# Optimization experiments

Hardware: AMD Instinct MI355X
Metric: run time of the kernel (lower is better)

Reference implementation:

```python
import jax, jax.numpy as jnp
import numpy as np

N = 62          # EEG channels (nodes per graph)
B = 512         # graphs in batch
K = 2           # SGConv propagation steps
F_IN = 128
H = 64
C = 3


def _complete_graph_edge_index():
    # edge e = g*N*N + i*N + j connects node g*N+i -> g*N+j,
    # matching edge_weight = Wsym.reshape(-1).repeat(B) ordering.
    base = np.arange(N)
    ii = np.tile(np.repeat(base, N), B)
    jj = np.tile(np.tile(base, N), B)
    off = np.repeat(np.arange(B) * N, N * N)
    return jnp.asarray(np.stack([off + ii, off + jj]).astype(np.int32))


def setup_inputs() -> dict:
    key = jax.random.key(0)
    ks = jax.random.split(key, 6)
    n_total = B * N
    x = jax.random.normal(ks[0], (n_total, F_IN), dtype=jnp.float32)
    edge_weight_tril = jax.random.normal(ks[1], (N * (N + 1) // 2,), dtype=jnp.float32)
    W1 = jax.random.normal(ks[2], (H, F_IN), dtype=jnp.float32) * (1.0 / np.sqrt(F_IN))
    b1 = jax.random.normal(ks[3], (H,), dtype=jnp.float32) * 0.01
    W2 = jax.random.normal(ks[4], (C, H), dtype=jnp.float32) * (1.0 / np.sqrt(H))
    b2 = jax.random.normal(ks[5], (C,), dtype=jnp.float32) * 0.01
    edge_index = _complete_graph_edge_index()
    batch = jnp.asarray(np.repeat(np.arange(B), N).astype(np.int32))
    return {"x": x, "edge_weight_tril": edge_weight_tril, "W1": W1, "b1": b1,
            "W2": W2, "b2": b2, "edge_index": edge_index, "batch": batch,
            "batch_size": B}


def reference(x, edge_weight_tril, W1, b1, W2, b2, edge_index, batch, batch_size):
    n_total = x.shape[0]
    # rebuild symmetric dense adjacency from lower-tri params
    xs, ys = np.tril_indices(N)
    Wm = jnp.zeros((N, N), dtype=x.dtype).at[xs, ys].set(edge_weight_tril)
    Wsym = Wm + Wm.T - jnp.diag(jnp.diag(Wm))
    ew = jnp.tile(Wsym.reshape(-1), batch_size)            # [B*N*N]

    row, col = edge_index[0], edge_index[1]
    # symmetric normalization (graph already contains self loops)
    deg = jax.ops.segment_sum(jnp.abs(ew), row, num_segments=n_total)
    dinv = jnp.where(deg > 0, deg ** -0.5, 0.0)
    norm = dinv[row] * ew * dinv[col]                      # [E]

    # K-step SGConv propagation: gather, scale, scatter-add
    h = x
    for _ in range(K):
        h = jax.ops.segment_sum(norm[:, None] * h[row], col, num_segments=n_total)

    h = jax.nn.relu(h @ W1.T + b1)                         # [n_total, H]
    pooled = jax.ops.segment_sum(h, batch, num_segments=batch_size)  # global_add_pool
    latent_v = pooled                                      # dropout in eval mode = identity
    logits = latent_v @ W2.T + b2
    logp = jax.nn.log_softmax(logits, axis=-1)
    return latent_v, logp
```

## Files before the change

### kernel.cpp

```cpp
#include <hip/hip_runtime.h>
#include <math.h>

#define NN  62
#define BGR 512
#define FIN 128
#define HD  64
#define NC  3

#define FMA4(dd, ss, vv) { (dd).x += (ss)*(vv).x; (dd).y += (ss)*(vv).y; (dd).z += (ss)*(vv).z; (dd).w += (ss)*(vv).w; }
#define RELUACC(pp, qq) { (pp).x += fmaxf((qq).x,0.f); (pp).y += fmaxf((qq).y,0.f); (pp).z += fmaxf((qq).z,0.f); (pp).w += fmaxf((qq).w,0.f); }


__global__ __launch_bounds__(256) void prep_kernel(const float* __restrict__ tril,
                                                   const float* __restrict__ W1,
                                                   float* __restrict__ A2g,
                                                   float* __restrict__ W1T) {
    __shared__ float LDSU[128 * 129];
    const int t = threadIdx.x;
    const int b = blockIdx.x;

    if (b == 4) {
        for (int e = t; e < HD * FIN; e += 256) {
            int h = e >> 7, f = e & 127;
            LDSU[h * 129 + f] = W1[e];
        }
        __syncthreads();
        for (int e = t; e < FIN * HD; e += 256) {
            int f = e >> 6, h = e & 63;
            W1T[e] = LDSU[h * 129 + f];
        }
        return;
    }

    float* trilS = LDSU;
    float* dinv  = LDSU + 1984;
    float* Ac    = LDSU + 2048;

    for (int e = t; e < NN * (NN + 1) / 2; e += 256) trilS[e] = tril[e];
    __syncthreads();
    if (t < NN) {
        float s = 0.f;
        for (int j = 0; j < NN; ++j) {
            int hi = max(t, j), lo = min(t, j);
            s += fabsf(trilS[hi * (hi + 1) / 2 + lo]);
        }
        dinv[t] = (s > 0.f) ? (1.0f / sqrtf(s)) : 0.f;
    }
    __syncthreads();
    for (int e = t; e < 64 * 64; e += 256) {
        int i = e >> 6, j = e & 63;
        float v = 0.f;
        if (i < NN && j < NN) {
            int hi = max(i, j), lo = min(i, j);
            v = dinv[i] * trilS[hi * (hi + 1) / 2 + lo] * dinv[j];
        }
        Ac[e] = v;
    }
    __syncthreads();
    {
        const int il = t >> 4, j4 = t & 15;
        const int i = 16 * b + il;
        const float4* Ac4 = (const float4*)Ac;
        float4 s4 = {0.f, 0.f, 0.f, 0.f};
        for (int k = 0; k < NN; ++k) {
            float a = Ac[i * 64 + k];
            float4 av = Ac4[k * 16 + j4];
            FMA4(s4, a, av);
        }
        ((float4*)A2g)[i * 16 + j4] = s4;
    }
}

__global__ __launch_bounds__(256) void gcn_fused(
    const float* __restrict__ x, const float* __restrict__ A2g,
    const float* __restrict__ W1T, const float* __restrict__ b1,
    const float* __restrict__ W2, const float* __restrict__ b2,
    float* __restrict__ out) {
    __shared__ float Xs[64 * 132];
    __shared__ float WU[128 * 64];

    const int t = threadIdx.x;
    const int g = blockIdx.x;
    const int iq = t >> 4;
    const int hq = t & 15;

    float4* Xs4 = (float4*)Xs;
    float4* WU4 = (float4*)WU;
    const float4* xg4  = (const float4*)(x + (size_t)g * NN * FIN);
    const float4* w1t4 = (const float4*)W1T;

    for (int e = t; e < 2048; e += 256) {
        int row = e >> 5, f4 = e & 31;
        float4 v = {0.f, 0.f, 0.f, 0.f};
        if (e < NN * 32) v = xg4[e];
        Xs4[row * 33 + f4] = v;
    }
    for (int e = t; e < 2048; e += 256) WU4[e] = w1t4[e];
    __syncthreads();

    float4 acc0 = {0,0,0,0}, acc1 = {0,0,0,0}, acc2 = {0,0,0,0}, acc3 = {0,0,0,0};
    for (int f4 = 0; f4 < 32; ++f4) {
        float4 xv0 = Xs4[(iq     ) * 33 + f4];
        float4 xv1 = Xs4[(iq + 16) * 33 + f4];
        float4 xv2 = Xs4[(iq + 32) * 33 + f4];
        float4 xv3 = Xs4[(iq + 48) * 33 + f4];
        float4 wv0 = WU4[(4 * f4 + 0) * 16 + hq];
        float4 wv1 = WU4[(4 * f4 + 1) * 16 + hq];
        float4 wv2 = WU4[(4 * f4 + 2) * 16 + hq];
        float4 wv3 = WU4[(4 * f4 + 3) * 16 + hq];
        FMA4(acc0, xv0.x, wv0); FMA4(acc0, xv0.y, wv1); FMA4(acc0, xv0.z, wv2); FMA4(acc0, xv0.w, wv3);
        FMA4(acc1, xv1.x, wv0); FMA4(acc1, xv1.y, wv1); FMA4(acc1, xv1.z, wv2); FMA4(acc1, xv1.w, wv3);
        FMA4(acc2, xv2.x, wv0); FMA4(acc2, xv2.y, wv1); FMA4(acc2, xv2.z, wv2); FMA4(acc2, xv2.w, wv3);
        FMA4(acc3, xv3.x, wv0); FMA4(acc3, xv3.y, wv1); FMA4(acc3, xv3.z, wv2); FMA4(acc3, xv3.w, wv3);
    }
    __syncthreads();

    float4* Yt4 = Xs4;
    Yt4[hq * 65 + iq     ] = acc0;
    Yt4[hq * 65 + iq + 16] = acc1;
    Yt4[hq * 65 + iq + 32] = acc2;
    Yt4[hq * 65 + iq + 48] = acc3;
    const float4* a2g4 = (const float4*)A2g;
    for (int e = t; e < 1024; e += 256) {
        int row = e >> 4, k4 = e & 15;
        WU4[row * 17 + k4] = a2g4[e];
    }
    __syncthreads();

    float4 b1v = ((const float4*)b1)[hq];
    float4 z0 = b1v, z1 = b1v, z2 = b1v, z3 = b1v;
    for (int j4 = 0; j4 < 16; ++j4) {
        float4 a0 = WU4[(iq     ) * 17 + j4];
        float4 a1 = WU4[(iq + 16) * 17 + j4];
        float4 a2 = WU4[(iq + 32) * 17 + j4];
        float4 a3 = WU4[(iq + 48) * 17 + j4];
        float4 y0 = Yt4[hq * 65 + 4 * j4 + 0];
        float4 y1 = Yt4[hq * 65 + 4 * j4 + 1];
        float4 y2 = Yt4[hq * 65 + 4 * j4 + 2];
        float4 y3 = Yt4[hq * 65 + 4 * j4 + 3];
        FMA4(z0, a0.x, y0); FMA4(z0, a0.y, y1); FMA4(z0, a0.z, y2); FMA4(z0, a0.w, y3);
        FMA4(z1, a1.x, y0); FMA4(z1, a1.y, y1); FMA4(z1, a1.z, y2); FMA4(z1, a1.w, y3);
        FMA4(z2, a2.x, y0); FMA4(z2, a2.y, y1); FMA4(z2, a2.z, y2); FMA4(z2, a2.w, y3);
        FMA4(z3, a3.x, y0); FMA4(z3, a3.y, y1); FMA4(z3, a3.z, y2); FMA4(z3, a3.w, y3);
    }

    float4 p = {0.f, 0.f, 0.f, 0.f};
    RELUACC(p, z0);
    RELUACC(p, z1);
    RELUACC(p, z2);
    if (iq < 14) RELUACC(p, z3);
    float* Pr = WU + 4352;
    Pr[(4 * hq + 0) * 17 + iq] = p.x;
    Pr[(4 * hq + 1) * 17 + iq] = p.y;
    Pr[(4 * hq + 2) * 17 + iq] = p.z;
    Pr[(4 * hq + 3) * 17 + iq] = p.w;
    __syncthreads();

    float* pooledS = WU + 5504;
    if (t < HD) {
        float s = 0.f;
        for (int q = 0; q < 16; ++q) s += Pr[t * 17 + q];
        out[(size_t)g * HD + t] = s;
        pooledS[t] = s;
    }
    __syncthreads();

    if (t < NC) {
        float lg[NC];
#pragma unroll
        for (int c = 0; c < NC; ++c) {
            float zz = b2[c];
            for (int h = 0; h < HD; ++h) zz += pooledS[h] * W2[c * HD + h];
            lg[c] = zz;
        }
        float m = fmaxf(lg[0], fmaxf(lg[1], lg[2]));
        float lse = m + logf(expf(lg[0] - m) + expf(lg[1] - m) + expf(lg[2] - m));
        out[(size_t)BGR * HD + (size_t)g * NC + t] = lg[t] - lse;
    }
}

extern "C" void kernel_launch(void* const* d_in, const int* in_sizes, int n_in,
                              void* d_out, int out_size, void* d_ws, size_t ws_size,
                              hipStream_t stream) {
    const float* x    = (const float*)d_in[0];
    const float* tril = (const float*)d_in[1];
    const float* W1   = (const float*)d_in[2];
    const float* b1   = (const float*)d_in[3];
    const float* W2   = (const float*)d_in[4];
    const float* b2   = (const float*)d_in[5];
    float* out  = (float*)d_out;
    float* A2g  = (float*)d_ws;
    float* W1T  = (float*)d_ws + 4096;

    prep_kernel<<<5, 256, 0, stream>>>(tril, W1, A2g, W1T);
    gcn_fused<<<BGR, 256, 0, stream>>>(x, A2g, W1T, b1, W2, b2, out);
}
```

Baseline: 106.2 us.

## Use bf16 split-precision MFMA for both per-graph matmuls

```diff
diff --git a/kernel.cpp b/kernel.cpp
--- a/kernel.cpp
+++ b/kernel.cpp
@@ -7,34 +7,43 @@
 #define HD  64
 #define NC  3
 
-#define FMA4(dd, ss, vv) { (dd).x += (ss)*(vv).x; (dd).y += (ss)*(vv).y; (dd).z += (ss)*(vv).z; (dd).w += (ss)*(vv).w; }
-#define RELUACC(pp, qq) { (pp).x += fmaxf((qq).x,0.f); (pp).y += fmaxf((qq).y,0.f); (pp).z += fmaxf((qq).z,0.f); (pp).w += fmaxf((qq).w,0.f); }
+typedef __attribute__((ext_vector_type(8))) short          bf16x8;
+typedef __attribute__((ext_vector_type(4))) float          f32x4;
+typedef __attribute__((ext_vector_type(4))) unsigned short us4;
+
+static __device__ __forceinline__ unsigned short f2bf(float f) {
+    union { float f; unsigned u; } v; v.f = f;
+    unsigned u = v.u;
+    return (unsigned short)((u + 0x7fffu + ((u >> 16) & 1u)) >> 16);
+}
+static __device__ __forceinline__ float bf2f(unsigned short h) {
+    union { unsigned u; float f; } v; v.u = ((unsigned)h) << 16;
+    return v.f;
+}
 
 
 __global__ __launch_bounds__(256) void prep_kernel(const float* __restrict__ tril,
                                                    const float* __restrict__ W1,
-                                                   float* __restrict__ A2g,
-                                                   float* __restrict__ W1T) {
-    __shared__ float LDSU[128 * 129];
+                                                   unsigned short* __restrict__ wsu) {
+    __shared__ float LDSF[1984 + 64 + 4096];
     const int t = threadIdx.x;
     const int b = blockIdx.x;
 
     if (b == 4) {
         for (int e = t; e < HD * FIN; e += 256) {
             int h = e >> 7, f = e & 127;
-            LDSU[h * 129 + f] = W1[e];
-        }
-        __syncthreads();
-        for (int e = t; e < FIN * HD; e += 256) {
-            int f = e >> 6, h = e & 63;
-            W1T[e] = LDSU[h * 129 + f];
+            float w = W1[e];
+            unsigned short hi = f2bf(w);
+            unsigned short lo = f2bf(w - bf2f(hi));
+            wsu[9216  + h * 136 + f] = hi;
+            wsu[17920 + h * 136 + f] = lo;
         }
         return;
     }
 
-    float* trilS = LDSU;
-    float* dinv  = LDSU + 1984;
-    float* Ac    = LDSU + 2048;
+    float* trilS = LDSF;
+    float* dinv  = LDSF + 1984;
+    float* Ac    = LDSF + 2048;
 
     for (int e = t; e < NN * (NN + 1) / 2; e += 256) trilS[e] = tril[e];
     __syncthreads();
@@ -65,101 +74,134 @@
         for (int k = 0; k < NN; ++k) {
             float a = Ac[i * 64 + k];
             float4 av = Ac4[k * 16 + j4];
-            FMA4(s4, a, av);
-        }
-        ((float4*)A2g)[i * 16 + j4] = s4;
+            s4.x += a * av.x; s4.y += a * av.y; s4.z += a * av.z; s4.w += a * av.w;
+        }
+        us4 hh, ll;
+        hh[0] = f2bf(s4.x); ll[0] = f2bf(s4.x - bf2f(hh[0]));
+        hh[1] = f2bf(s4.y); ll[1] = f2bf(s4.y - bf2f(hh[1]));
+        hh[2] = f2bf(s4.z); ll[2] = f2bf(s4.z - bf2f(hh[2]));
+        hh[3] = f2bf(s4.w); ll[3] = f2bf(s4.w - bf2f(hh[3]));
+        *(us4*)&wsu[       i * 72 + 4 * j4] = hh;
+        *(us4*)&wsu[4608 + i * 72 + 4 * j4] = ll;
     }
 }
 
 __global__ __launch_bounds__(256) void gcn_fused(
-    const float* __restrict__ x, const float* __restrict__ A2g,
-    const float* __restrict__ W1T, const float* __restrict__ b1,
-    const float* __restrict__ W2, const float* __restrict__ b2,
-    float* __restrict__ out) {
-    __shared__ float Xs[64 * 132];
-    __shared__ float WU[128 * 64];
+    const float* __restrict__ x, const unsigned short* __restrict__ wsu,
+    const float* __restrict__ b1, const float* __restrict__ W2,
+    const float* __restrict__ b2, float* __restrict__ out) {
+    __shared__ unsigned short SH[34816];
+    __shared__ float TAIL[64 * 17 + 64 + 64];
+    float* partial = TAIL;
+    float* pooledS = TAIL + 1088;
+    float* b1S     = TAIL + 1152;
 
     const int t = threadIdx.x;
     const int g = blockIdx.x;
-    const int iq = t >> 4;
-    const int hq = t & 15;
-
-    float4* Xs4 = (float4*)Xs;
-    float4* WU4 = (float4*)WU;
-    const float4* xg4  = (const float4*)(x + (size_t)g * NN * FIN);
-    const float4* w1t4 = (const float4*)W1T;
-
+    const int lane = t & 63, wv = t >> 6, quad = lane >> 4, l15 = lane & 15;
+
+    if (t < 16) *(float4*)&b1S[4 * t] = ((const float4*)b1)[t];
+
+    const float4* xg4 = (const float4*)(x + (size_t)g * NN * FIN);
     for (int e = t; e < 2048; e += 256) {
-        int row = e >> 5, f4 = e & 31;
+        int row = e >> 5, k4 = e & 31;
         float4 v = {0.f, 0.f, 0.f, 0.f};
-        if (e < NN * 32) v = xg4[e];
-        Xs4[row * 33 + f4] = v;
-    }
-    for (int e = t; e < 2048; e += 256) WU4[e] = w1t4[e];
-    __syncthreads();
-
-    float4 acc0 = {0,0,0,0}, acc1 = {0,0,0,0}, acc2 = {0,0,0,0}, acc3 = {0,0,0,0};
-    for (int f4 = 0; f4 < 32; ++f4) {
-        float4 xv0 = Xs4[(iq     ) * 33 + f4];
-        float4 xv1 = Xs4[(iq + 16) * 33 + f4];
-        float4 xv2 = Xs4[(iq + 32) * 33 + f4];
-        float4 xv3 = Xs4[(iq + 48) * 33 + f4];
-        float4 wv0 = WU4[(4 * f4 + 0) * 16 + hq];
-        float4 wv1 = WU4[(4 * f4 + 1) * 16 + hq];
-        float4 wv2 = WU4[(4 * f4 + 2) * 16 + hq];
-        float4 wv3 = WU4[(4 * f4 + 3) * 16 + hq];
-        FMA4(acc0, xv0.x, wv0); FMA4(acc0, xv0.y, wv1); FMA4(acc0, xv0.z, wv2); FMA4(acc0, xv0.w, wv3);
-        FMA4(acc1, xv1.x, wv0); FMA4(acc1, xv1.y, wv1); FMA4(acc1, xv1.z, wv2); FMA4(acc1, xv1.w, wv3);
-        FMA4(acc2, xv2.x, wv0); FMA4(acc2, xv2.y, wv1); FMA4(acc2, xv2.z, wv2); FMA4(acc2, xv2.w, wv3);
-        FMA4(acc3, xv3.x, wv0); FMA4(acc3, xv3.y, wv1); FMA4(acc3, xv3.z, wv2); FMA4(acc3, xv3.w, wv3);
-    }
-    __syncthreads();
-
-    float4* Yt4 = Xs4;
-    Yt4[hq * 65 + iq     ] = acc0;
-    Yt4[hq * 65 + iq + 16] = acc1;
-    Yt4[hq * 65 + iq + 32] = acc2;
-    Yt4[hq * 65 + iq + 48] = acc3;
-    const float4* a2g4 = (const float4*)A2g;
-    for (int e = t; e < 1024; e += 256) {
-        int row = e >> 4, k4 = e & 15;
-        WU4[row * 17 + k4] = a2g4[e];
-    }
-    __syncthreads();
-
-    float4 b1v = ((const float4*)b1)[hq];
-    float4 z0 = b1v, z1 = b1v, z2 = b1v, z3 = b1v;
-    for (int j4 = 0; j4 < 16; ++j4) {
-        float4 a0 = WU4[(iq     ) * 17 + j4];
-        float4 a1 = WU4[(iq + 16) * 17 + j4];
-        float4 a2 = WU4[(iq + 32) * 17 + j4];
-        float4 a3 = WU4[(iq + 48) * 17 + j4];
-        float4 y0 = Yt4[hq * 65 + 4 * j4 + 0];
-        float4 y1 = Yt4[hq * 65 + 4 * j4 + 1];
-        float4 y2 = Yt4[hq * 65 + 4 * j4 + 2];
-        float4 y3 = Yt4[hq * 65 + 4 * j4 + 3];
-        FMA4(z0, a0.x, y0); FMA4(z0, a0.y, y1); FMA4(z0, a0.z, y2); FMA4(z0, a0.w, y3);
-        FMA4(z1, a1.x, y0); FMA4(z1, a1.y, y1); FMA4(z1, a1.z, y2); FMA4(z1, a1.w, y3);
-        FMA4(z2, a2.x, y0); FMA4(z2, a2.y, y1); FMA4(z2, a2.z, y2); FMA4(z2, a2.w, y3);
-        FMA4(z3, a3.x, y0); FMA4(z3, a3.y, y1); FMA4(z3, a3.z, y2); FMA4(z3, a3.w, y3);
-    }
-
-    float4 p = {0.f, 0.f, 0.f, 0.f};
-    RELUACC(p, z0);
-    RELUACC(p, z1);
-    RELUACC(p, z2);
-    if (iq < 14) RELUACC(p, z3);
-    float* Pr = WU + 4352;
-    Pr[(4 * hq + 0) * 17 + iq] = p.x;
-    Pr[(4 * hq + 1) * 17 + iq] = p.y;
-    Pr[(4 * hq + 2) * 17 + iq] = p.z;
-    Pr[(4 * hq + 3) * 17 + iq] = p.w;
-    __syncthreads();
-
-    float* pooledS = WU + 5504;
+        if (e < 1984) v = xg4[e];
+        us4 hh, ll;
+        hh[0] = f2bf(v.x); ll[0] = f2bf(v.x - bf2f(hh[0]));
+        hh[1] = f2bf(v.y); ll[1] = f2bf(v.y - bf2f(hh[1]));
+        hh[2] = f2bf(v.z); ll[2] = f2bf(v.z - bf2f(hh[2]));
+        hh[3] = f2bf(v.w); ll[3] = f2bf(v.w - bf2f(hh[3]));
+        *(us4*)&SH[       row * 136 + k4 * 4] = hh;
+        *(us4*)&SH[8704 + row * 136 + k4 * 4] = ll;
+    }
+    {
+        const float4* wsrc = (const float4*)(wsu + 9216);
+        for (int e = t; e < 2176; e += 256) *(float4*)&SH[17408 + e * 8] = wsrc[e];
+    }
+    __syncthreads();
+
+    f32x4 y0 = {0,0,0,0}, y1 = {0,0,0,0}, y2 = {0,0,0,0}, y3 = {0,0,0,0};
+    {
+        const int arow = (16 * wv + l15) * 136 + quad * 8;
+#pragma unroll
+        for (int c = 0; c < 4; ++c) {
+            bf16x8 ahi = *(bf16x8*)&SH[arow + c * 32];
+            bf16x8 alo = *(bf16x8*)&SH[8704 + arow + c * 32];
+#define P1TILE(ACC, NT) { \
+            int bo = (16 * NT + l15) * 136 + quad * 8 + c * 32; \
+            bf16x8 bhi = *(bf16x8*)&SH[17408 + bo]; \
+            bf16x8 blo = *(bf16x8*)&SH[26112 + bo]; \
+            ACC = __builtin_amdgcn_mfma_f32_16x16x32_bf16(ahi, bhi, ACC, 0, 0, 0); \
+            ACC = __builtin_amdgcn_mfma_f32_16x16x32_bf16(ahi, blo, ACC, 0, 0, 0); \
+            ACC = __builtin_amdgcn_mfma_f32_16x16x32_bf16(alo, bhi, ACC, 0, 0, 0); \
+            ACC = __builtin_amdgcn_mfma_f32_16x16x32_bf16(alo, blo, ACC, 0, 0, 0); }
+            P1TILE(y0, 0) P1TILE(y1, 1) P1TILE(y2, 2) P1TILE(y3, 3)
+#undef P1TILE
+        }
+    }
+    __syncthreads();
+
+    {
+        const int mbase = 16 * wv + quad * 4;
+#define YTW(ACC, NT) { \
+        int n = 16 * NT + l15; \
+        us4 hh, ll; \
+        hh[0] = f2bf(ACC[0]); ll[0] = f2bf(ACC[0] - bf2f(hh[0])); \
+        hh[1] = f2bf(ACC[1]); ll[1] = f2bf(ACC[1] - bf2f(hh[1])); \
+        hh[2] = f2bf(ACC[2]); ll[2] = f2bf(ACC[2] - bf2f(hh[2])); \
+        hh[3] = f2bf(ACC[3]); ll[3] = f2bf(ACC[3] - bf2f(hh[3])); \
+        *(us4*)&SH[       n * 72 + mbase] = hh; \
+        *(us4*)&SH[4608 + n * 72 + mbase] = ll; }
+        YTW(y0, 0) YTW(y1, 1) YTW(y2, 2) YTW(y3, 3)
+#undef YTW
+    }
+    {
+        const float4* a2src = (const float4*)wsu;
+        for (int e = t; e < 1152; e += 256) *(float4*)&SH[9216 + e * 8] = a2src[e];
+    }
+    __syncthreads();
+
+    f32x4 z0 = {0,0,0,0}, z1 = {0,0,0,0}, z2 = {0,0,0,0}, z3 = {0,0,0,0};
+    {
+        const int arow = 9216 + (16 * wv + l15) * 72 + quad * 8;
+#pragma unroll
+        for (int c = 0; c < 2; ++c) {
+            bf16x8 ahi = *(bf16x8*)&SH[arow + c * 32];
+            bf16x8 alo = *(bf16x8*)&SH[4608 + arow + c * 32];
+#define P2TILE(ACC, NT) { \
+            int bo = (16 * NT + l15) * 72 + quad * 8 + c * 32; \
+            bf16x8 bhi = *(bf16x8*)&SH[bo]; \
+            bf16x8 blo = *(bf16x8*)&SH[4608 + bo]; \
+            ACC = __builtin_amdgcn_mfma_f32_16x16x32_bf16(ahi, bhi, ACC, 0, 0, 0); \
+            ACC = __builtin_amdgcn_mfma_f32_16x16x32_bf16(ahi, blo, ACC, 0, 0, 0); \
+            ACC = __builtin_amdgcn_mfma_f32_16x16x32_bf16(alo, bhi, ACC, 0, 0, 0); \
+            ACC = __builtin_amdgcn_mfma_f32_16x16x32_bf16(alo, blo, ACC, 0, 0, 0); }
+            P2TILE(z0, 0) P2TILE(z1, 1) P2TILE(z2, 2) P2TILE(z3, 3)
+#undef P2TILE
+        }
+    }
+
+    {
+        const int mbase = 16 * wv + quad * 4;
+        const int slot = 4 * wv + quad;
+#define POOL(ACC, NT) { \
+        int n = 16 * NT + l15; \
+        float bn = b1S[n]; \
+        float p = 0.f; \
+        if (mbase + 0 < 62) p += fmaxf(ACC[0] + bn, 0.f); \
+        if (mbase + 1 < 62) p += fmaxf(ACC[1] + bn, 0.f); \
+        if (mbase + 2 < 62) p += fmaxf(ACC[2] + bn, 0.f); \
+        if (mbase + 3 < 62) p += fmaxf(ACC[3] + bn, 0.f); \
+        partial[n * 17 + slot] = p; }
+        POOL(z0, 0) POOL(z1, 1) POOL(z2, 2) POOL(z3, 3)
+#undef POOL
+    }
+    __syncthreads();
+
     if (t < HD) {
         float s = 0.f;
-        for (int q = 0; q < 16; ++q) s += Pr[t * 17 + q];
+        for (int q = 0; q < 16; ++q) s += partial[t * 17 + q];
         out[(size_t)g * HD + t] = s;
         pooledS[t] = s;
     }
@@ -188,10 +230,9 @@
     const float* b1   = (const float*)d_in[3];
     const float* W2   = (const float*)d_in[4];
     const float* b2   = (const float*)d_in[5];
-    float* out  = (float*)d_out;
-    float* A2g  = (float*)d_ws;
-    float* W1T  = (float*)d_ws + 4096;
-
-    prep_kernel<<<5, 256, 0, stream>>>(tril, W1, A2g, W1T);
-    gcn_fused<<<BGR, 256, 0, stream>>>(x, A2g, W1T, b1, W2, b2, out);
-}
+    float* out = (float*)d_out;
+    unsigned short* wsu = (unsigned short*)d_ws;
+
+    prep_kernel<<<5, 256, 0, stream>>>(tril, W1, wsu);
+    gcn_fused<<<BGR, 256, 0, stream>>>(x, wsu, b1, W2, b2, out);
+}
```

Measured after the change: 104.4 us. No clear change (-1.6%).
